# Optimization experiments

Hardware: AMD Instinct MI355X
Metric: run time of the kernel (lower is better)

The kernel has to match this reference:

```python
import math
import jax, jax.numpy as jnp
import numpy as np

B, S, HID = 2, 2048, 3072
NH, HD = 32, 96            # num_heads, head_dim; num_kv_heads == num_heads (n_rep = 1)
OP = NH * HD + 2 * (NH * HD)  # 9216


def _rope_tables(seq_len, head_dim, theta=10000.0):
    inv_freq = 1.0 / (theta ** (np.arange(0, head_dim, 2, dtype=np.float32) / head_dim))
    t = np.arange(seq_len, dtype=np.float32)
    freqs = np.outer(t, inv_freq)                      # [S, HD/2]
    emb = np.concatenate([freqs, freqs], axis=-1)      # [S, HD]
    return jnp.asarray(np.cos(emb)), jnp.asarray(np.sin(emb))


def setup_inputs() -> dict:
    key = jax.random.key(0)
    k1, k2, k3 = jax.random.split(key, 3)
    hidden_states = jax.random.normal(k1, (B, S, HID), dtype=jnp.float32)
    cos, sin = _rope_tables(S, HD)
    # additive causal mask [B, 1, S, S]
    neg = jnp.finfo(jnp.float32).min
    causal = jnp.where(jnp.tril(jnp.ones((S, S), dtype=bool)), 0.0, neg)
    attention_mask = jnp.broadcast_to(causal[None, None], (B, 1, S, S)).astype(jnp.float32)
    Wqkv = jax.random.normal(k2, (HID, OP), dtype=jnp.float32) * (HID ** -0.5)
    Wo = jax.random.normal(k3, (NH * HD, HID), dtype=jnp.float32) * ((NH * HD) ** -0.5)
    return {"hidden_states": hidden_states, "cos": cos, "sin": sin,
            "attention_mask": attention_mask, "Wqkv": Wqkv, "Wo": Wo}


def _rotate_half(x):
    x1, x2 = jnp.split(x, 2, axis=-1)
    return jnp.concatenate([-x2, x1], axis=-1)


def reference(hidden_states, cos, sin, attention_mask, Wqkv, Wo):
    bsz, q_len, _ = hidden_states.shape
    qkv = hidden_states @ Wqkv                                    # [B,S,OP]
    q, k, v = jnp.split(qkv, [NH * HD, 2 * NH * HD], axis=-1)
    # [B,S,H*D] -> [B,H,S,D]
    to_bhsd = lambda t: t.reshape(bsz, q_len, NH, HD).transpose(0, 2, 1, 3)
    q, k, v = to_bhsd(q), to_bhsd(k), to_bhsd(v)
    c = cos[None, None]                                           # [1,1,S,D]
    s = sin[None, None]
    q = q * c + _rotate_half(q) * s
    k = k * c + _rotate_half(k) * s
    # num_key_value_groups == 1, so repeat_kv is identity.
    scores = jnp.einsum('bhqd,bhkd->bhqk', q, k) / math.sqrt(HD)  # [B,H,S,S]
    scores = scores + attention_mask
    attn = jax.nn.softmax(scores.astype(jnp.float32), axis=-1).astype(v.dtype)
    # dropout p=0.0 / eval -> identity
    out = jnp.einsum('bhqk,bhkd->bhqd', attn, v)                  # [B,H,S,D]
    out = out.transpose(0, 2, 1, 3).reshape(bsz, q_len, NH * HD)
    return out @ Wo                                               # [B,S,HID]
```

## Files before the change

kernel.cpp:

```cpp
#include <hip/hip_runtime.h>

typedef __bf16  bf16x8 __attribute__((ext_vector_type(8)));
typedef float   f32x4  __attribute__((ext_vector_type(4)));
typedef float   f32x16 __attribute__((ext_vector_type(16)));
typedef short   i16x8  __attribute__((ext_vector_type(8)));
typedef unsigned short u16x4 __attribute__((ext_vector_type(4)));
typedef unsigned int   u32x4 __attribute__((ext_vector_type(4)));

__device__ __forceinline__ float bf2f(unsigned short u) {
    union { unsigned int i; float f; } v; v.i = ((unsigned int)u) << 16; return v.f;
}
__device__ __forceinline__ unsigned short f2bf(float f) {
    union { float f; unsigned int i; } v; v.f = f;
    unsigned int r = v.i + 0x7FFFu + ((v.i >> 16) & 1u);
    return (unsigned short)(r >> 16);
}
__device__ __forceinline__ unsigned packbf(float lo, float hi) {
    return (unsigned)f2bf(lo) | ((unsigned)f2bf(hi) << 16);
}
__device__ __forceinline__ void gload_lds16(const void* g, void* l) {
    __builtin_amdgcn_global_load_lds(
        (const __attribute__((address_space(1))) void*)g,
        (__attribute__((address_space(3))) void*)l, 16, 0, 0);
}
__device__ __forceinline__ void pswap(unsigned &x, unsigned &y) {
#if __has_builtin(__builtin_amdgcn_permlane32_swap)
    auto r = __builtin_amdgcn_permlane32_swap((int)x, (int)y, false, false);
    x = (unsigned)r[0]; y = (unsigned)r[1];
#else
    unsigned nx = (threadIdx.x & 32) ? (unsigned)__shfl_xor((int)y, 32) : x;
    unsigned ny = (threadIdx.x & 32) ? y : (unsigned)__shfl_xor((int)x, 32);
    x = nx; y = ny;
#endif
}
__device__ __forceinline__ float partner_f(float v, int hi) {
    unsigned x = __builtin_bit_cast(unsigned, v), y = x;
    pswap(x, y);
    return __builtin_bit_cast(float, hi ? x : y);
}

__global__ __launch_bounds__(256) void cast_f32_bf16(
    const float* __restrict__ in, unsigned short* __restrict__ out, int n8)
{
    int i = blockIdx.x * 256 + threadIdx.x;
    if (i >= n8) return;
    const f32x4* p = (const f32x4*)(in + (long)i * 8);
    f32x4 a = p[0], b = p[1];
    i16x8 o;
    o[0]=(short)f2bf(a[0]); o[1]=(short)f2bf(a[1]); o[2]=(short)f2bf(a[2]); o[3]=(short)f2bf(a[3]);
    o[4]=(short)f2bf(b[0]); o[5]=(short)f2bf(b[1]); o[6]=(short)f2bf(b[2]); o[7]=(short)f2bf(b[3]);
    *(i16x8*)(out + (long)i * 8) = o;
}

__global__ __launch_bounds__(256) void transpose_cast(
    const float* __restrict__ in, unsigned short* __restrict__ out, int R, int C)
{
    __shared__ float tile[64][65];
    int c0 = blockIdx.x * 64, r0 = blockIdx.y * 64;
    int tx = threadIdx.x & 63, ty = threadIdx.x >> 6;
#pragma unroll
    for (int i = 0; i < 64; i += 4)
        tile[ty + i][tx] = in[(long)(r0 + ty + i) * C + c0 + tx];
    __syncthreads();
#pragma unroll
    for (int i = 0; i < 64; i += 4)
        out[(long)(c0 + ty + i) * R + r0 + tx] = f2bf(tile[tx][ty + i]);
}

template <int MODE>
__global__ __launch_bounds__(256) void gemm_bt(
    const unsigned short* __restrict__ A, const unsigned short* __restrict__ B,
    int K, int N,
    unsigned short* __restrict__ Qo, unsigned short* __restrict__ Ko,
    unsigned short* __restrict__ Vo, float* __restrict__ Cf)
{
    __shared__ unsigned short Al[128 * 64];
    __shared__ unsigned short Bl[128 * 64];
    const int t = threadIdx.x;
    const int w = t >> 6, l = t & 63, lhi = l >> 4, llo = l & 15;
    const int m0 = blockIdx.x * 128, n0 = blockIdx.y * 128;
    const int wmo = (w >> 1) << 6, wno = (w & 1) << 6;

    const unsigned short* ag[4];
    const unsigned short* bg[4];
#pragma unroll
    for (int i = 0; i < 4; ++i) {
        int j = i * 256 + t;
        int row = j >> 3;
        int c = (j & 7) ^ (row & 7);
        ag[i] = A + (long)(m0 + row) * K + c * 8;
        bg[i] = B + (long)(n0 + row) * K + c * 8;
    }

    f32x4 acc[4][4] = {};
    const int nkt = K >> 6;
    for (int kt = 0; kt < nkt; ++kt) {
        __syncthreads();
#pragma unroll
        for (int i = 0; i < 4; ++i) {
            gload_lds16(ag[i] + kt * 64, &Al[(i * 256 + (w << 6)) * 8]);
            gload_lds16(bg[i] + kt * 64, &Bl[(i * 256 + (w << 6)) * 8]);
        }
        __syncthreads();
#pragma unroll
        for (int kf = 0; kf < 2; ++kf) {
            bf16x8 af[4], bfv[4];
#pragma unroll
            for (int mi = 0; mi < 4; ++mi) {
                int row = wmo + mi * 16 + llo;
                int cc = (kf * 4 + lhi) ^ (row & 7);
                af[mi] = __builtin_bit_cast(bf16x8, *(const i16x8*)&Al[row * 64 + cc * 8]);
            }
#pragma unroll
            for (int ni = 0; ni < 4; ++ni) {
                int row = wno + ni * 16 + llo;
                int cc = (kf * 4 + lhi) ^ (row & 7);
                bfv[ni] = __builtin_bit_cast(bf16x8, *(const i16x8*)&Bl[row * 64 + cc * 8]);
            }
#pragma unroll
            for (int mi = 0; mi < 4; ++mi)
#pragma unroll
                for (int ni = 0; ni < 4; ++ni)
                    acc[mi][ni] = __builtin_amdgcn_mfma_f32_16x16x32_bf16(
                        af[mi], bfv[ni], acc[mi][ni], 0, 0, 0);
        }
    }

#pragma unroll
    for (int mi = 0; mi < 4; ++mi) {
        int s0g = m0 + wmo + mi * 16 + (lhi << 2);
#pragma unroll
        for (int ni = 0; ni < 4; ++ni) {
            int gcol = n0 + wno + ni * 16 + llo;
            if (MODE == 1) {
#pragma unroll
                for (int r = 0; r < 4; ++r)
                    Cf[(long)(s0g + r) * N + gcol] = acc[mi][ni][r];
            } else {
                int seg = gcol / 3072;
                int cc2 = gcol - seg * 3072;
                int h = cc2 / 96, d = cc2 - h * 96;
                int b = s0g >> 11, s = s0g & 2047;
                long bh = (long)((b << 5) + h);
                if (seg == 2) {
                    u16x4 pv;
#pragma unroll
                    for (int r = 0; r < 4; ++r) pv[r] = f2bf(acc[mi][ni][r]);
                    *(u16x4*)(Vo + (bh * 96 + d) * 2048 + s) = pv;
                } else {
                    unsigned short* dst = seg ? Ko : Qo;
#pragma unroll
                    for (int r = 0; r < 4; ++r)
                        dst[(bh * 2048 + s + r) * 96 + d] = f2bf(acc[mi][ni][r]);
                }
            }
        }
    }
}

__global__ __launch_bounds__(256) void rope_kernel(
    unsigned short* __restrict__ Qb, unsigned short* __restrict__ Kb,
    const float* __restrict__ cosT, const float* __restrict__ sinT)
{
    int i = blockIdx.x * 256 + threadIdx.x;
    int d6 = i % 6;
    int sbh = i / 6;
    int s = sbh & 2047;
    long base = (long)sbh * 96 + d6 * 8;
    const f32x4* cp = (const f32x4*)(cosT + s * 96 + d6 * 8);
    const f32x4* sp = (const f32x4*)(sinT + s * 96 + d6 * 8);
    f32x4 c0 = cp[0], c1 = cp[1], s0 = sp[0], s1 = sp[1];
    float cv[8] = {c0[0],c0[1],c0[2],c0[3],c1[0],c1[1],c1[2],c1[3]};
    float sv[8] = {s0[0],s0[1],s0[2],s0[3],s1[0],s1[1],s1[2],s1[3]};
    i16x8 qlo = *(i16x8*)(Qb + base), qhi = *(i16x8*)(Qb + base + 48);
    i16x8 klo = *(i16x8*)(Kb + base), khi = *(i16x8*)(Kb + base + 48);
    i16x8 qlo2, qhi2, klo2, khi2;
#pragma unroll
    for (int j = 0; j < 8; ++j) {
        float ql = bf2f((unsigned short)qlo[j]), qh = bf2f((unsigned short)qhi[j]);
        float kl = bf2f((unsigned short)klo[j]), kh = bf2f((unsigned short)khi[j]);
        qlo2[j] = (short)f2bf(ql * cv[j] - qh * sv[j]);
        qhi2[j] = (short)f2bf(qh * cv[j] + ql * sv[j]);
        klo2[j] = (short)f2bf(kl * cv[j] - kh * sv[j]);
        khi2[j] = (short)f2bf(kh * cv[j] + kl * sv[j]);
    }
    *(i16x8*)(Qb + base) = qlo2; *(i16x8*)(Qb + base + 48) = qhi2;
    *(i16x8*)(Kb + base) = klo2; *(i16x8*)(Kb + base + 48) = khi2;
}

__global__ __launch_bounds__(256, 2) void attn_fwd(
    const unsigned short* __restrict__ Q, const unsigned short* __restrict__ Kt,
    const unsigned short* __restrict__ Vg, unsigned short* __restrict__ O)
{
    __shared__ __align__(16) unsigned short Kl[2][64 * 128];
    __shared__ __align__(16) unsigned short Vl[2][96 * 64];
    const int t = threadIdx.x;
    const int w = t >> 6, l = t & 63;
    const int l31 = l & 31, hi = l >> 5, l7 = l & 7;
    const int bh = blockIdx.x;
    constexpr float C2 = 0.14724450f;

    const unsigned short* Kg  = Kt + (long)bh * 2048 * 96;
    const unsigned short* Vgb = Vg + (long)bh * 96 * 2048;

#define STAGE_KV(buf, tile)                                                        \
    {                                                                              \
        _Pragma("unroll")                                                          \
        for (int i_ = 0; i_ < 4; ++i_) {                                           \
            int row_ = (w << 4) + (i_ << 2) + (l >> 4);                            \
            gload_lds16(Kg + ((long)(tile) * 64 + row_) * 96 +                     \
                            (((l & 15) ^ (row_ & 7)) << 3),                        \
                        &Kl[buf][((w << 4) + (i_ << 2)) << 7]);                    \
        }                                                                          \
        _Pragma("unroll")                                                          \
        for (int i_ = 0; i_ < 3; ++i_) {                                           \
            int row_ = w * 24 + (i_ << 3) + (l >> 3);                              \
            gload_lds16(Vgb + (long)row_ * 2048 + (tile) * 64 +                    \
                            ((l7 ^ (row_ & 7)) << 3),                              \
                        &Vl[buf][(w * 24 + (i_ << 3)) << 6]);                      \
        }                                                                          \
    }

    const int b = bh >> 5, h = bh & 31;

    for (int pass = 0; pass < 2; ++pass) {
        const int qb = pass ? 7 - (int)blockIdx.y : (int)blockIdx.y;
        const int q0b = qb << 8;
        const int nkv = 4 * qb + 4;
        const int kd = 4 * qb + w;

        bf16x8 qf[2][6];
#pragma unroll
        for (int qs = 0; qs < 2; ++qs) {
            const unsigned short* qp =
                Q + ((long)bh * 2048 + q0b + (w << 6) + (qs << 5) + l31) * 96 + (hi << 3);
#pragma unroll
            for (int ks = 0; ks < 6; ++ks)
                qf[qs][ks] = __builtin_bit_cast(bf16x8, *(const i16x8*)(qp + ks * 16));
        }

        f32x16 oa[2][3] = {};
        float m_r[2] = {-1e30f, -1e30f};
        float l_r[2] = {0.f, 0.f};

        STAGE_KV(0, 0);
        STAGE_KV(1, 1);

        for (int kt = 0; kt < nkv; ++kt) {
            const int cb = kt & 1;
            if (kt < nkv - 1) asm volatile("s_waitcnt vmcnt(7)" ::: "memory");
            else              asm volatile("s_waitcnt vmcnt(0)" ::: "memory");
            __builtin_amdgcn_s_barrier();

            if (kt <= kd) {
                bf16x8 pf[2][4];
#pragma unroll
                for (int qs = 0; qs < 2; ++qs) {
                    f32x16 s0 = {}, s1 = {};
                    __builtin_amdgcn_s_setprio(1);
#pragma unroll
                    for (int ks = 0; ks < 6; ++ks) {
                        bf16x8 k0 = __builtin_bit_cast(bf16x8, *(const i16x8*)
                            &Kl[cb][(l31 << 7) + ((((ks << 1) + hi) ^ l7) << 3)]);
                        bf16x8 k1 = __builtin_bit_cast(bf16x8, *(const i16x8*)
                            &Kl[cb][((32 + l31) << 7) + ((((ks << 1) + hi) ^ l7) << 3)]);
                        s0 = __builtin_amdgcn_mfma_f32_32x32x16_bf16(k0, qf[qs][ks], s0, 0, 0, 0);
                        s1 = __builtin_amdgcn_mfma_f32_32x32x16_bf16(k1, qf[qs][ks], s1, 0, 0, 0);
                    }
                    __builtin_amdgcn_s_setprio(0);

                    if (kt == kd) {
                        const int ql = (qs << 5) + l31;
#pragma unroll
                        for (int r = 0; r < 16; ++r) {
                            int kvl = (r & 3) + ((r >> 2) << 3) + (hi << 2);
                            if (kvl > ql)      s0[r] = -1e30f;
                            if (kvl + 32 > ql) s1[r] = -1e30f;
                        }
                    }
                    float px = s0[0];
#pragma unroll
                    for (int r = 1; r < 16; ++r) px = fmaxf(px, s0[r]);
#pragma unroll
                    for (int r = 0; r < 16; ++r) px = fmaxf(px, s1[r]);
                    px = fmaxf(px, partner_f(px, hi));
                    if (__any(px > m_r[qs] + 54.0f)) {
                        float mnew = fmaxf(m_r[qs], px);
                        float scl = exp2f((m_r[qs] - mnew) * C2);
                        l_r[qs] *= scl;
#pragma unroll
                        for (int tt = 0; tt < 3; ++tt)
#pragma unroll
                            for (int r = 0; r < 16; ++r) oa[qs][tt][r] *= scl;
                        m_r[qs] = mnew;
                    }
                    const float mC = m_r[qs] * C2;
                    float ls = 0.f;
#pragma unroll
                    for (int r = 0; r < 16; ++r) {
                        s0[r] = exp2f(fmaf(s0[r], C2, -mC));
                        s1[r] = exp2f(fmaf(s1[r], C2, -mC));
                        ls += s0[r] + s1[r];
                    }
                    l_r[qs] += ls;
#pragma unroll
                    for (int s = 0; s < 4; ++s) {
                        const f32x16& pv = (s >= 2) ? s1 : s0;
                        const int bb = (s & 1) << 3;
                        unsigned d0 = packbf(pv[bb + 0], pv[bb + 1]);
                        unsigned d2 = packbf(pv[bb + 4], pv[bb + 5]);
                        pswap(d0, d2);
                        unsigned d1 = packbf(pv[bb + 2], pv[bb + 3]);
                        unsigned d3 = packbf(pv[bb + 6], pv[bb + 7]);
                        pswap(d1, d3);
                        pf[qs][s] = __builtin_bit_cast(bf16x8, (u32x4){d0, d1, d2, d3});
                    }
                }
                __builtin_amdgcn_s_setprio(1);
#pragma unroll
                for (int s = 0; s < 4; ++s) {
#pragma unroll
                    for (int tt = 0; tt < 3; ++tt) {
                        bf16x8 vf = __builtin_bit_cast(bf16x8, *(const i16x8*)
                            &Vl[cb][((tt << 5) + l31) * 64 + ((((s << 1) + hi) ^ l7) << 3)]);
                        oa[0][tt] = __builtin_amdgcn_mfma_f32_32x32x16_bf16(vf, pf[0][s], oa[0][tt], 0, 0, 0);
                        oa[1][tt] = __builtin_amdgcn_mfma_f32_32x32x16_bf16(vf, pf[1][s], oa[1][tt], 0, 0, 0);
                    }
                }
                __builtin_amdgcn_s_setprio(0);
            }

            asm volatile("s_waitcnt lgkmcnt(0)" ::: "memory");
            __builtin_amdgcn_s_barrier();
            if (kt + 2 < nkv) STAGE_KV(cb, kt + 2);
        }

#pragma unroll
        for (int qs = 0; qs < 2; ++qs) {
            float lt = l_r[qs] + partner_f(l_r[qs], hi);
            float inv = 1.0f / lt;
            const int qg = q0b + (w << 6) + (qs << 5) + l31;
            unsigned short* ob = O + ((long)(b * 2048 + qg)) * 3072 + h * 96;
#pragma unroll
            for (int tt = 0; tt < 3; ++tt)
#pragma unroll
                for (int qd = 0; qd < 4; ++qd) {
                    u16x4 o4;
#pragma unroll
                    for (int j = 0; j < 4; ++j)
                        o4[j] = f2bf(oa[qs][tt][(qd << 2) + j] * inv);
                    *(u16x4*)(ob + (tt << 5) + (qd << 3) + (hi << 2)) = o4;
                }
        }
    }
#undef STAGE_KV
}

extern "C" void kernel_launch(void* const* d_in, const int* in_sizes, int n_in,
                              void* d_out, int out_size, void* d_ws, size_t ws_size,
                              hipStream_t stream) {
    const float* hidden = (const float*)d_in[0];
    const float* cosT   = (const float*)d_in[1];
    const float* sinT   = (const float*)d_in[2];
    const float* Wqkv   = (const float*)d_in[4];
    const float* Wo     = (const float*)d_in[5];
    float* out = (float*)d_out;

    char* ws = (char*)d_ws;
    unsigned short* Ah  = (unsigned short*)ws;
    unsigned short* WqT = (unsigned short*)(ws + 25165824);
    unsigned short* Qb  = (unsigned short*)(ws + 25165824 + 56623104);
    unsigned short* Kb  = Qb + 12582912;
    unsigned short* Vb  = Kb + 12582912;

    cast_f32_bf16<<<6144, 256, 0, stream>>>(hidden, Ah, 1572864);
    transpose_cast<<<dim3(144, 48), 256, 0, stream>>>(Wqkv, WqT, 3072, 9216);
    gemm_bt<0><<<dim3(32, 72), 256, 0, stream>>>(Ah, WqT, 3072, 9216, Qb, Kb, Vb, nullptr);
    transpose_cast<<<dim3(48, 48), 256, 0, stream>>>(Wo, WqT, 3072, 3072);
    rope_kernel<<<3072, 256, 0, stream>>>(Qb, Kb, cosT, sinT);
    attn_fwd<<<dim3(64, 4), 256, 0, stream>>>(Qb, Kb, Vb, Ah);
    gemm_bt<1><<<dim3(32, 24), 256, 0, stream>>>(Ah, WqT, 3072, 3072,
                                                 nullptr, nullptr, nullptr, out);
}
```

Measured before the change: 615.5 us.

## Halve attention Q tile to 128 rows and double grid blocks

Each attention block now processes a 128-row query tile with one 32-row subtile per wave, instead of 256 rows with two subtiles per wave. The grid doubles to 512 blocks, and causal pairing becomes qt with 15−qt. This aims to raise occupancy and balance work across CUs while cutting per-wave registers. The cost is that each staged K/V tile is reused by half as many query rows, which increases LDS and global K/V traffic per flop.

```diff
diff --git a/kernel.cpp b/kernel.cpp
--- a/kernel.cpp
+++ b/kernel.cpp
@@ -224,24 +224,22 @@
     const int b = bh >> 5, h = bh & 31;
 
     for (int pass = 0; pass < 2; ++pass) {
-        const int qb = pass ? 7 - (int)blockIdx.y : (int)blockIdx.y;
-        const int q0b = qb << 8;
-        const int nkv = 4 * qb + 4;
-        const int kd = 4 * qb + w;
-
-        bf16x8 qf[2][6];
-#pragma unroll
-        for (int qs = 0; qs < 2; ++qs) {
+        const int qt = pass ? 15 - (int)blockIdx.y : (int)blockIdx.y;
+        const int q0b = qt << 7;
+        const int nkv = 2 * qt + 2;
+        const int kd  = 2 * qt + (w >> 1);
+
+        bf16x8 qf[6];
+        {
             const unsigned short* qp =
-                Q + ((long)bh * 2048 + q0b + (w << 6) + (qs << 5) + l31) * 96 + (hi << 3);
+                Q + ((long)bh * 2048 + q0b + (w << 5) + l31) * 96 + (hi << 3);
 #pragma unroll
             for (int ks = 0; ks < 6; ++ks)
-                qf[qs][ks] = __builtin_bit_cast(bf16x8, *(const i16x8*)(qp + ks * 16));
-        }
-
-        f32x16 oa[2][3] = {};
-        float m_r[2] = {-1e30f, -1e30f};
-        float l_r[2] = {0.f, 0.f};
+                qf[ks] = __builtin_bit_cast(bf16x8, *(const i16x8*)(qp + ks * 16));
+        }
+
+        f32x16 oa[3] = {};
+        float m_r = -1e30f, l_r = 0.f;
 
         STAGE_KV(0, 0);
         STAGE_KV(1, 1);
@@ -253,68 +251,68 @@
             __builtin_amdgcn_s_barrier();
 
             if (kt <= kd) {
-                bf16x8 pf[2][4];
-#pragma unroll
-                for (int qs = 0; qs < 2; ++qs) {
-                    f32x16 s0 = {}, s1 = {};
-                    __builtin_amdgcn_s_setprio(1);
-#pragma unroll
-                    for (int ks = 0; ks < 6; ++ks) {
-                        bf16x8 k0 = __builtin_bit_cast(bf16x8, *(const i16x8*)
-                            &Kl[cb][(l31 << 7) + ((((ks << 1) + hi) ^ l7) << 3)]);
-                        bf16x8 k1 = __builtin_bit_cast(bf16x8, *(const i16x8*)
-                            &Kl[cb][((32 + l31) << 7) + ((((ks << 1) + hi) ^ l7) << 3)]);
-                        s0 = __builtin_amdgcn_mfma_f32_32x32x16_bf16(k0, qf[qs][ks], s0, 0, 0, 0);
-                        s1 = __builtin_amdgcn_mfma_f32_32x32x16_bf16(k1, qf[qs][ks], s1, 0, 0, 0);
-                    }
-                    __builtin_amdgcn_s_setprio(0);
-
-                    if (kt == kd) {
-                        const int ql = (qs << 5) + l31;
-#pragma unroll
-                        for (int r = 0; r < 16; ++r) {
-                            int kvl = (r & 3) + ((r >> 2) << 3) + (hi << 2);
-                            if (kvl > ql)      s0[r] = -1e30f;
-                            if (kvl + 32 > ql) s1[r] = -1e30f;
+                f32x16 s0 = {}, s1 = {};
+                __builtin_amdgcn_s_setprio(1);
+#pragma unroll
+                for (int ks = 0; ks < 6; ++ks) {
+                    bf16x8 k0 = __builtin_bit_cast(bf16x8, *(const i16x8*)
+                        &Kl[cb][(l31 << 7) + ((((ks << 1) + hi) ^ l7) << 3)]);
+                    bf16x8 k1 = __builtin_bit_cast(bf16x8, *(const i16x8*)
+                        &Kl[cb][((32 + l31) << 7) + ((((ks << 1) + hi) ^ l7) << 3)]);
+                    s0 = __builtin_amdgcn_mfma_f32_32x32x16_bf16(k0, qf[ks], s0, 0, 0, 0);
+                    s1 = __builtin_amdgcn_mfma_f32_32x32x16_bf16(k1, qf[ks], s1, 0, 0, 0);
+                }
+                __builtin_amdgcn_s_setprio(0);
+
+                if (kt == kd) {
+#pragma unroll
+                    for (int r = 0; r < 16; ++r) {
+                        int kvl = (r & 3) + ((r >> 2) << 3) + (hi << 2);
+                        if (w & 1) {
+                            if (kvl > l31) s1[r] = -1e30f;
+                        } else {
+                            if (kvl > l31) s0[r] = -1e30f;
+                            s1[r] = -1e30f;
                         }
                     }
-                    float px = s0[0];
-#pragma unroll
-                    for (int r = 1; r < 16; ++r) px = fmaxf(px, s0[r]);
-#pragma unroll
-                    for (int r = 0; r < 16; ++r) px = fmaxf(px, s1[r]);
-                    px = fmaxf(px, partner_f(px, hi));
-                    if (__any(px > m_r[qs] + 54.0f)) {
-                        float mnew = fmaxf(m_r[qs], px);
-                        float scl = exp2f((m_r[qs] - mnew) * C2);
-                        l_r[qs] *= scl;
-#pragma unroll
-                        for (int tt = 0; tt < 3; ++tt)
-#pragma unroll
-                            for (int r = 0; r < 16; ++r) oa[qs][tt][r] *= scl;
-                        m_r[qs] = mnew;
-                    }
-                    const float mC = m_r[qs] * C2;
-                    float ls = 0.f;
-#pragma unroll
-                    for (int r = 0; r < 16; ++r) {
-                        s0[r] = exp2f(fmaf(s0[r], C2, -mC));
-                        s1[r] = exp2f(fmaf(s1[r], C2, -mC));
-                        ls += s0[r] + s1[r];
-                    }
-                    l_r[qs] += ls;
-#pragma unroll
-                    for (int s = 0; s < 4; ++s) {
-                        const f32x16& pv = (s >= 2) ? s1 : s0;
-                        const int bb = (s & 1) << 3;
-                        unsigned d0 = packbf(pv[bb + 0], pv[bb + 1]);
-                        unsigned d2 = packbf(pv[bb + 4], pv[bb + 5]);
-                        pswap(d0, d2);
-                        unsigned d1 = packbf(pv[bb + 2], pv[bb + 3]);
-                        unsigned d3 = packbf(pv[bb + 6], pv[bb + 7]);
-                        pswap(d1, d3);
-                        pf[qs][s] = __builtin_bit_cast(bf16x8, (u32x4){d0, d1, d2, d3});
-                    }
+                }
+                float px = s0[0];
+#pragma unroll
+                for (int r = 1; r < 16; ++r) px = fmaxf(px, s0[r]);
+#pragma unroll
+                for (int r = 0; r < 16; ++r) px = fmaxf(px, s1[r]);
+                px = fmaxf(px, partner_f(px, hi));
+                if (__any(px > m_r + 54.0f)) {
+                    float mnew = fmaxf(m_r, px);
+                    float scl = exp2f((m_r - mnew) * C2);
+                    l_r *= scl;
+#pragma unroll
+                    for (int tt = 0; tt < 3; ++tt)
+#pragma unroll
+                        for (int r = 0; r < 16; ++r) oa[tt][r] *= scl;
+                    m_r = mnew;
+                }
+                const float mC = m_r * C2;
+                float ls = 0.f;
+#pragma unroll
+                for (int r = 0; r < 16; ++r) {
+                    s0[r] = exp2f(fmaf(s0[r], C2, -mC));
+                    s1[r] = exp2f(fmaf(s1[r], C2, -mC));
+                    ls += s0[r] + s1[r];
+                }
+                l_r += ls;
+                bf16x8 pf[4];
+#pragma unroll
+                for (int s = 0; s < 4; ++s) {
+                    const f32x16& pv = (s >= 2) ? s1 : s0;
+                    const int bb = (s & 1) << 3;
+                    unsigned d0 = packbf(pv[bb + 0], pv[bb + 1]);
+                    unsigned d2 = packbf(pv[bb + 4], pv[bb + 5]);
+                    pswap(d0, d2);
+                    unsigned d1 = packbf(pv[bb + 2], pv[bb + 3]);
+                    unsigned d3 = packbf(pv[bb + 6], pv[bb + 7]);
+                    pswap(d1, d3);
+                    pf[s] = __builtin_bit_cast(bf16x8, (u32x4){d0, d1, d2, d3});
                 }
                 __builtin_amdgcn_s_setprio(1);
 #pragma unroll
@@ -323,8 +321,7 @@
                     for (int tt = 0; tt < 3; ++tt) {
                         bf16x8 vf = __builtin_bit_cast(bf16x8, *(const i16x8*)
                             &Vl[cb][((tt << 5) + l31) * 64 + ((((s << 1) + hi) ^ l7) << 3)]);
-                        oa[0][tt] = __builtin_amdgcn_mfma_f32_32x32x16_bf16(vf, pf[0][s], oa[0][tt], 0, 0, 0);
-                        oa[1][tt] = __builtin_amdgcn_mfma_f32_32x32x16_bf16(vf, pf[1][s], oa[1][tt], 0, 0, 0);
+                        oa[tt] = __builtin_amdgcn_mfma_f32_32x32x16_bf16(vf, pf[s], oa[tt], 0, 0, 0);
                     }
                 }
                 __builtin_amdgcn_s_setprio(0);
@@ -335,11 +332,10 @@
             if (kt + 2 < nkv) STAGE_KV(cb, kt + 2);
         }
 
-#pragma unroll
-        for (int qs = 0; qs < 2; ++qs) {
-            float lt = l_r[qs] + partner_f(l_r[qs], hi);
+        {
+            float lt = l_r + partner_f(l_r, hi);
             float inv = 1.0f / lt;
-            const int qg = q0b + (w << 6) + (qs << 5) + l31;
+            const int qg = q0b + (w << 5) + l31;
             unsigned short* ob = O + ((long)(b * 2048 + qg)) * 3072 + h * 96;
 #pragma unroll
             for (int tt = 0; tt < 3; ++tt)
@@ -348,7 +344,7 @@
                     u16x4 o4;
 #pragma unroll
                     for (int j = 0; j < 4; ++j)
-                        o4[j] = f2bf(oa[qs][tt][(qd << 2) + j] * inv);
+                        o4[j] = f2bf(oa[tt][(qd << 2) + j] * inv);
                     *(u16x4*)(ob + (tt << 5) + (qd << 3) + (hi << 2)) = o4;
                 }
         }
@@ -378,7 +374,7 @@
     gemm_bt<0><<<dim3(32, 72), 256, 0, stream>>>(Ah, WqT, 3072, 9216, Qb, Kb, Vb, nullptr);
     transpose_cast<<<dim3(48, 48), 256, 0, stream>>>(Wo, WqT, 3072, 3072);
     rope_kernel<<<3072, 256, 0, stream>>>(Qb, Kb, cosT, sinT);
-    attn_fwd<<<dim3(64, 4), 256, 0, stream>>>(Qb, Kb, Vb, Ah);
+    attn_fwd<<<dim3(64, 8), 256, 0, stream>>>(Qb, Kb, Vb, Ah);
     gemm_bt<1><<<dim3(32, 24), 256, 0, stream>>>(Ah, WqT, 3072, 3072,
                                                  nullptr, nullptr, nullptr, out);
 }
```

Result: faster. 515.4 us (-16.3%).
